# Optimization experiments

Measured on AMD Instinct MI355X. Metric: run time of the kernel, lower is better.

The kernel has to match this reference:

```python
import jax, jax.numpy as jnp
import numpy as np

ALPHA = 0.95  # membrane/filter decay
BETA = 0.9    # output decay
NB_HIDDEN, NB_OUTPUTS, NB_STEPS, BATCH = 256, 16, 2000, 128


def setup_inputs() -> dict:
    key = jax.random.key(0)
    k1, k2 = jax.random.split(key)
    inputs = jax.random.normal(k1, (BATCH, NB_STEPS, NB_HIDDEN), dtype=jnp.float32)
    weight_scale = 0.2
    output_weights = jax.random.normal(k2, (NB_HIDDEN, NB_OUTPUTS), dtype=jnp.float32) * (
        weight_scale / np.sqrt(NB_HIDDEN)
    )
    return {"inputs": inputs, "output_weights": output_weights}


def reference(inputs, output_weights):
    # inputs: [B, T, H], output_weights: [H, O]
    h2 = jnp.einsum("bth,ho->bto", inputs, output_weights)  # [B, T, O]
    B, T, O = h2.shape
    dtype = h2.dtype

    def step(carry, h_t):
        flt, out = carry
        new_flt = ALPHA * flt + h_t        # uses old flt
        new_out = BETA * out + flt         # uses OLD flt (matches torch code)
        return (new_flt, new_out), new_out

    init = (jnp.zeros((B, O), dtype), jnp.zeros((B, O), dtype))
    _, outs = jax.lax.scan(step, init, jnp.swapaxes(h2, 0, 1))  # outs: [T, B, O]
    out_rec = jnp.concatenate(
        [jnp.zeros((B, 1, O), dtype), jnp.swapaxes(outs, 0, 1)], axis=1
    )  # [B, T+1, O], first slot is the initial zero state (out_rec = [out0] + ...)
    return out_rec
```

## Files before the change

### kernel.cpp

```cpp
#include <hip/hip_runtime.h>


constexpr int B_ = 128, T_ = 2000, H_ = 256, O_ = 16;
constexpr int TOUT = T_ + 1;
constexpr int CHUNKS = 8, CL = 250;
constexpr int HC = 32;
constexpr int SSTR = 36;
constexpr int PAD = 20;
constexpr float ALPHA = 0.95f, BETA = 0.9f;
constexpr float INV_AB = 20.0f;
constexpr float L2A = -0.07400058144377693f;
constexpr float L2B = -0.15200309344504997f;

__global__ __launch_bounds__(256, 4)
void h2scan_kernel(const float* __restrict__ in, const float* __restrict__ W,
                   float* __restrict__ out, float* __restrict__ ws) {
    __shared__ float buf[CL * SSTR];
    const int tid = threadIdx.x;
    const int b = blockIdx.x >> 3;
    const int j = blockIdx.x & 7;

    const float* inb = in + ((size_t)b * T_ + (size_t)j * CL) * H_;
    const int row = (tid < CL) ? tid : 0;

    float acc[16];
#pragma unroll
    for (int o = 0; o < 16; ++o) acc[o] = 0.f;

    for (int c = 0; c < CHUNKS; ++c) {
#pragma unroll
        for (int it = 0; it < 8; ++it) {
            const int f = it * 256 + tid;
            if (f < CL * 8) {
                const int r = f >> 3, q = f & 7;
                const float4 v =
                    *(const float4*)(inb + (size_t)r * H_ + c * HC + 4 * q);
                *(float4*)&buf[r * SSTR + 4 * q] = v;
            }
        }
        __syncthreads();

        float x[HC];
#pragma unroll
        for (int q = 0; q < 8; ++q) {
            const float4 v = *(const float4*)&buf[row * SSTR + 4 * q];
            x[4 * q + 0] = v.x; x[4 * q + 1] = v.y;
            x[4 * q + 2] = v.z; x[4 * q + 3] = v.w;
        }
        const float* __restrict__ Wc = W + c * HC * O_;
#pragma unroll
        for (int hh = 0; hh < HC; ++hh) {
            const float xv = x[hh];
#pragma unroll
            for (int o = 0; o < 16; ++o)
                acc[o] = fmaf(xv, Wc[hh * 16 + o], acc[o]);
        }
        __syncthreads();
    }

    if (tid < CL) {
        float4* tp = (float4*)&buf[tid * PAD];
        tp[0] = make_float4(acc[0],  acc[1],  acc[2],  acc[3]);
        tp[1] = make_float4(acc[4],  acc[5],  acc[6],  acc[7]);
        tp[2] = make_float4(acc[8],  acc[9],  acc[10], acc[11]);
        tp[3] = make_float4(acc[12], acc[13], acc[14], acc[15]);
    }
    __syncthreads();

    if (tid < O_) {
        float flt = 0.f, oo = 0.f;
        float* col = &buf[tid];
#pragma unroll 5
        for (int t = 0; t < CL; ++t) {
            const float h = col[t * PAD];
            const float no = fmaf(BETA, oo, flt);
            flt = fmaf(ALPHA, flt, h);
            col[t * PAD] = no;
            oo = no;
        }
        float* wp = ws + ((size_t)(b * O_ + tid) * CHUNKS + j) * 2;
        wp[0] = flt;
        wp[1] = oo;
        if (j == 0) out[(size_t)b * TOUT * O_ + tid] = 0.f;
    }
    __syncthreads();

    const size_t obase = ((size_t)b * TOUT + (size_t)j * CL + 1) * O_;
    for (int e = tid; e < CL * O_; e += 256)
        out[obase + e] = buf[(e >> 4) * PAD + (e & 15)];
}

__global__ __launch_bounds__(256)
void fixup_kernel(float* __restrict__ out, const float* __restrict__ ws) {
    const int blk = blockIdx.x;
    const int b = blk >> 3;
    const int j = blk & 7;
    if (j == 0) return;

    __shared__ float f0s[O_], o0s[O_];
    const int tid = threadIdx.x;
    if (tid < O_) {
        const float* wp = ws + ((size_t)(b * O_ + tid) * CHUNKS) * 2;
        float f = 0.f, oacc = 0.f;
        for (int m = 0; m < j; ++m) {
            const float k  = (float)((j - 1 - m) * CL);
            const float a  = exp2f(k * L2A);
            const float bb = exp2f(k * L2B);
            const float g  = (a - bb) * INV_AB;
            const float sf = wp[m * 2 + 0];
            const float so = wp[m * 2 + 1];
            f    = fmaf(a, sf, f);
            oacc = fmaf(g, sf, fmaf(bb, so, oacc));
        }
        f0s[tid] = f;
        o0s[tid] = oacc;
    }
    __syncthreads();

    const size_t rowbase = ((size_t)b * TOUT + (size_t)j * CL + 1) * O_;
    for (int e = tid; e < CL * O_; e += 256) {
        const int tloc = e >> 4;
        const int o = e & 15;
        const float k  = (float)(tloc + 1);
        const float a  = exp2f(k * L2A);
        const float bb = exp2f(k * L2B);
        const float g  = (a - bb) * INV_AB;
        out[rowbase + e] = fmaf(g, f0s[o], fmaf(bb, o0s[o], out[rowbase + e]));
    }
}

extern "C" void kernel_launch(void* const* d_in, const int* in_sizes, int n_in,
                              void* d_out, int out_size, void* d_ws, size_t ws_size,
                              hipStream_t stream) {
    const float* in = (const float*)d_in[0];
    const float* W  = (const float*)d_in[1];
    float* out = (float*)d_out;
    float* ws  = (float*)d_ws;

    h2scan_kernel<<<dim3(B_ * CHUNKS), dim3(256), 0, stream>>>(in, W, out, ws);
    fixup_kernel<<<dim3(B_ * CHUNKS), dim3(256), 0, stream>>>(out, ws);
}
```

Baseline: 73.36 us.

## Prefetch next input chunk into registers and vectorize output stores

Loads for the next 32-column input chunk are issued into registers before the current chunk's FMA loop, so global memory latency overlaps with compute instead of stalling after each barrier. The staging loop drops the per-iteration bounds check and keeps a single guarded tail. Output writes in the scan kernel and read-modify-writes in the fixup kernel now use float4 accesses. The prefetch buffer adds 32 VGPRs, which may reduce occupancy under launch_bounds(256,4).

Result: slower. 143.5 us (+95.5%).

```diff
diff --git a/kernel.cpp b/kernel.cpp
--- a/kernel.cpp
+++ b/kernel.cpp
@@ -22,38 +22,61 @@
 
     const float* inb = in + ((size_t)b * T_ + (size_t)j * CL) * H_;
     const int row = (tid < CL) ? tid : 0;
+    const bool tail_ok = (tid < 208);
 
     float acc[16];
 #pragma unroll
     for (int o = 0; o < 16; ++o) acc[o] = 0.f;
 
+    float4 pf[8];
+#pragma unroll
+    for (int it = 0; it < 7; ++it) {
+        const int f = it * 256 + tid;
+        pf[it] = *(const float4*)(inb + (size_t)(f >> 3) * H_ + 4 * (f & 7));
+    }
+    {
+        const int f7 = 7 * 256 + tid;
+        if (tail_ok)
+            pf[7] = *(const float4*)(inb + (size_t)(f7 >> 3) * H_ + 4 * (f7 & 7));
+    }
+
     for (int c = 0; c < CHUNKS; ++c) {
 #pragma unroll
-        for (int it = 0; it < 8; ++it) {
+        for (int it = 0; it < 7; ++it) {
             const int f = it * 256 + tid;
-            if (f < CL * 8) {
-                const int r = f >> 3, q = f & 7;
-                const float4 v =
-                    *(const float4*)(inb + (size_t)r * H_ + c * HC + 4 * q);
-                *(float4*)&buf[r * SSTR + 4 * q] = v;
-            }
+            *(float4*)&buf[(f >> 3) * SSTR + 4 * (f & 7)] = pf[it];
+        }
+        if (tail_ok) {
+            const int f7 = 7 * 256 + tid;
+            *(float4*)&buf[(f7 >> 3) * SSTR + 4 * (f7 & 7)] = pf[7];
         }
         __syncthreads();
 
-        float x[HC];
+        if (c + 1 < CHUNKS) {
+            const float* inc = inb + (c + 1) * HC;
+#pragma unroll
+            for (int it = 0; it < 7; ++it) {
+                const int f = it * 256 + tid;
+                pf[it] = *(const float4*)(inc + (size_t)(f >> 3) * H_ + 4 * (f & 7));
+            }
+            const int f7 = 7 * 256 + tid;
+            if (tail_ok)
+                pf[7] = *(const float4*)(inc + (size_t)(f7 >> 3) * H_ + 4 * (f7 & 7));
+        }
+
+        const float* __restrict__ Wc = W + c * HC * O_;
 #pragma unroll
         for (int q = 0; q < 8; ++q) {
             const float4 v = *(const float4*)&buf[row * SSTR + 4 * q];
-            x[4 * q + 0] = v.x; x[4 * q + 1] = v.y;
-            x[4 * q + 2] = v.z; x[4 * q + 3] = v.w;
-        }
-        const float* __restrict__ Wc = W + c * HC * O_;
+            const float xv[4] = {v.x, v.y, v.z, v.w};
 #pragma unroll
-        for (int hh = 0; hh < HC; ++hh) {
-            const float xv = x[hh];
+            for (int e = 0; e < 4; ++e) {
+                const float x = xv[e];
+                const float* wrow = Wc + (4 * q + e) * 16;
 #pragma unroll
-            for (int o = 0; o < 16; ++o)
-                acc[o] = fmaf(xv, Wc[hh * 16 + o], acc[o]);
+                for (int o = 0; o < 16; ++o)
+                    acc[o] = fmaf(x, wrow[o], acc[o]);
+            }
         }
         __syncthreads();
     }
@@ -85,9 +108,16 @@
     }
     __syncthreads();
 
-    const size_t obase = ((size_t)b * TOUT + (size_t)j * CL + 1) * O_;
-    for (int e = tid; e < CL * O_; e += 256)
-        out[obase + e] = buf[(e >> 4) * PAD + (e & 15)];
+    float4* ob = (float4*)(out + ((size_t)b * TOUT + (size_t)j * CL + 1) * O_);
+#pragma unroll
+    for (int it = 0; it < 4; ++it) {
+        const int e4 = it * 256 + tid;
+        if (e4 < CL * 4) {
+            const int tloc = e4 >> 2, qo = 4 * (e4 & 3);
+            const float* tp = &buf[tloc * PAD + qo];
+            ob[e4] = make_float4(tp[0], tp[1], tp[2], tp[3]);
+        }
+    }
 }
 
 __global__ __launch_bounds__(256)
@@ -117,15 +147,23 @@
     }
     __syncthreads();
 
-    const size_t rowbase = ((size_t)b * TOUT + (size_t)j * CL + 1) * O_;
-    for (int e = tid; e < CL * O_; e += 256) {
-        const int tloc = e >> 4;
-        const int o = e & 15;
-        const float k  = (float)(tloc + 1);
-        const float a  = exp2f(k * L2A);
-        const float bb = exp2f(k * L2B);
-        const float g  = (a - bb) * INV_AB;
-        out[rowbase + e] = fmaf(g, f0s[o], fmaf(bb, o0s[o], out[rowbase + e]));
+    float4* ob = (float4*)(out + ((size_t)b * TOUT + (size_t)j * CL + 1) * O_);
+#pragma unroll
+    for (int it = 0; it < 4; ++it) {
+        const int e4 = it * 256 + tid;
+        if (e4 < CL * 4) {
+            const int tloc = e4 >> 2, qo = 4 * (e4 & 3);
+            const float k  = (float)(tloc + 1);
+            const float a  = exp2f(k * L2A);
+            const float bb = exp2f(k * L2B);
+            const float g  = (a - bb) * INV_AB;
+            float4 v = ob[e4];
+            v.x = fmaf(g, f0s[qo + 0], fmaf(bb, o0s[qo + 0], v.x));
+            v.y = fmaf(g, f0s[qo + 1], fmaf(bb, o0s[qo + 1], v.y));
+            v.z = fmaf(g, f0s[qo + 2], fmaf(bb, o0s[qo + 2], v.z));
+            v.w = fmaf(g, f0s[qo + 3], fmaf(bb, o0s[qo + 3], v.w));
+            ob[e4] = v;
+        }
     }
 }
 
```

## Fuse scan and fixup kernels via decoupled look-back across chunk blocks

Applied to the files above, without the earlier changes.

Merges the fixup kernel into the scan kernel. Each chunk block publishes its final (flt, out) state as a 64-bit atomic with release semantics, then spin-waits on the states of earlier chunks of the same batch row. It applies the carry correction from shared memory before writing its output with float4 stores. This removes a second kernel launch and a full read-modify-write pass over the output. In exchange it adds a memset of the workspace and spin-waits that rely on earlier blocks being scheduled first.

After: 137.1 us. +86.9%, slower.

```diff
diff --git a/kernel.cpp b/kernel.cpp
--- a/kernel.cpp
+++ b/kernel.cpp
@@ -11,11 +11,13 @@
 constexpr float INV_AB = 20.0f;
 constexpr float L2A = -0.07400058144377693f;
 constexpr float L2B = -0.15200309344504997f;
+constexpr unsigned long long SENTINEL = 0xFFFFFFFFFFFFFFFFull;
 
 __global__ __launch_bounds__(256, 4)
-void h2scan_kernel(const float* __restrict__ in, const float* __restrict__ W,
-                   float* __restrict__ out, float* __restrict__ ws) {
+void fused_kernel(const float* __restrict__ in, const float* __restrict__ W,
+                  float* __restrict__ out, unsigned long long* __restrict__ ws) {
     __shared__ float buf[CL * SSTR];
+    __shared__ float f0s[O_], o0s[O_];
     const int tid = threadIdx.x;
     const int b = blockIdx.x >> 3;
     const int j = blockIdx.x & 7;
@@ -40,20 +42,19 @@
         }
         __syncthreads();
 
-        float x[HC];
+        const float* __restrict__ Wc = W + c * HC * O_;
 #pragma unroll
         for (int q = 0; q < 8; ++q) {
             const float4 v = *(const float4*)&buf[row * SSTR + 4 * q];
-            x[4 * q + 0] = v.x; x[4 * q + 1] = v.y;
-            x[4 * q + 2] = v.z; x[4 * q + 3] = v.w;
-        }
-        const float* __restrict__ Wc = W + c * HC * O_;
+            const float xv[4] = {v.x, v.y, v.z, v.w};
 #pragma unroll
-        for (int hh = 0; hh < HC; ++hh) {
-            const float xv = x[hh];
+            for (int e = 0; e < 4; ++e) {
+                const float x = xv[e];
+                const float* wrow = Wc + (4 * q + e) * 16;
 #pragma unroll
-            for (int o = 0; o < 16; ++o)
-                acc[o] = fmaf(xv, Wc[hh * 16 + o], acc[o]);
+                for (int o = 0; o < 16; ++o)
+                    acc[o] = fmaf(x, wrow[o], acc[o]);
+            }
         }
         __syncthreads();
     }
@@ -78,37 +79,25 @@
             col[t * PAD] = no;
             oo = no;
         }
-        float* wp = ws + ((size_t)(b * O_ + tid) * CHUNKS + j) * 2;
-        wp[0] = flt;
-        wp[1] = oo;
+        const unsigned long long pay =
+            ((unsigned long long)__float_as_uint(oo) << 32) | __float_as_uint(flt);
+        __hip_atomic_store(&ws[(size_t)(b * CHUNKS + j) * O_ + tid], pay,
+                           __ATOMIC_RELEASE, __HIP_MEMORY_SCOPE_AGENT);
         if (j == 0) out[(size_t)b * TOUT * O_ + tid] = 0.f;
-    }
-    __syncthreads();
 
-    const size_t obase = ((size_t)b * TOUT + (size_t)j * CL + 1) * O_;
-    for (int e = tid; e < CL * O_; e += 256)
-        out[obase + e] = buf[(e >> 4) * PAD + (e & 15)];
-}
-
-__global__ __launch_bounds__(256)
-void fixup_kernel(float* __restrict__ out, const float* __restrict__ ws) {
-    const int blk = blockIdx.x;
-    const int b = blk >> 3;
-    const int j = blk & 7;
-    if (j == 0) return;
-
-    __shared__ float f0s[O_], o0s[O_];
-    const int tid = threadIdx.x;
-    if (tid < O_) {
-        const float* wp = ws + ((size_t)(b * O_ + tid) * CHUNKS) * 2;
         float f = 0.f, oacc = 0.f;
         for (int m = 0; m < j; ++m) {
+            unsigned long long v;
+            do {
+                v = __hip_atomic_load(&ws[(size_t)(b * CHUNKS + m) * O_ + tid],
+                                      __ATOMIC_ACQUIRE, __HIP_MEMORY_SCOPE_AGENT);
+            } while (v == SENTINEL);
+            const float sf = __uint_as_float((unsigned)(v & 0xFFFFFFFFu));
+            const float so = __uint_as_float((unsigned)(v >> 32));
             const float k  = (float)((j - 1 - m) * CL);
             const float a  = exp2f(k * L2A);
             const float bb = exp2f(k * L2B);
             const float g  = (a - bb) * INV_AB;
-            const float sf = wp[m * 2 + 0];
-            const float so = wp[m * 2 + 1];
             f    = fmaf(a, sf, f);
             oacc = fmaf(g, sf, fmaf(bb, so, oacc));
         }
@@ -117,15 +106,24 @@
     }
     __syncthreads();
 
-    const size_t rowbase = ((size_t)b * TOUT + (size_t)j * CL + 1) * O_;
-    for (int e = tid; e < CL * O_; e += 256) {
-        const int tloc = e >> 4;
-        const int o = e & 15;
-        const float k  = (float)(tloc + 1);
-        const float a  = exp2f(k * L2A);
-        const float bb = exp2f(k * L2B);
-        const float g  = (a - bb) * INV_AB;
-        out[rowbase + e] = fmaf(g, f0s[o], fmaf(bb, o0s[o], out[rowbase + e]));
+    float4* ob = (float4*)(out + ((size_t)b * TOUT + (size_t)j * CL + 1) * O_);
+#pragma unroll
+    for (int it = 0; it < 4; ++it) {
+        const int e4 = it * 256 + tid;
+        if (e4 < CL * 4) {
+            const int tloc = e4 >> 2, qo = 4 * (e4 & 3);
+            const float k  = (float)(tloc + 1);
+            const float a  = exp2f(k * L2A);
+            const float bb = exp2f(k * L2B);
+            const float g  = (a - bb) * INV_AB;
+            const float* tp = &buf[tloc * PAD + qo];
+            float4 v;
+            v.x = fmaf(g, f0s[qo + 0], fmaf(bb, o0s[qo + 0], tp[0]));
+            v.y = fmaf(g, f0s[qo + 1], fmaf(bb, o0s[qo + 1], tp[1]));
+            v.z = fmaf(g, f0s[qo + 2], fmaf(bb, o0s[qo + 2], tp[2]));
+            v.w = fmaf(g, f0s[qo + 3], fmaf(bb, o0s[qo + 3], tp[3]));
+            ob[e4] = v;
+        }
     }
 }
 
@@ -135,8 +133,8 @@
     const float* in = (const float*)d_in[0];
     const float* W  = (const float*)d_in[1];
     float* out = (float*)d_out;
-    float* ws  = (float*)d_ws;
+    unsigned long long* ws = (unsigned long long*)d_ws;
 
-    h2scan_kernel<<<dim3(B_ * CHUNKS), dim3(256), 0, stream>>>(in, W, out, ws);
-    fixup_kernel<<<dim3(B_ * CHUNKS), dim3(256), 0, stream>>>(out, ws);
+    hipMemsetAsync(d_ws, 0xFF, (size_t)B_ * CHUNKS * O_ * 8, stream);
+    fused_kernel<<<dim3(B_ * CHUNKS), dim3(256), 0, stream>>>(in, W, out, ws);
 }
```
